# Kernel optimization log

Hardware: AMD Instinct MI355X
Metric: run time of the kernel (lower is better)

Reference implementation:

```python
import jax, jax.numpy as jnp
import numpy as np

INPUT_SIZE = 1024
HEAD_SIZE = 64


def setup_inputs() -> dict:
    key = jax.random.key(0)
    kx, kk, kq, kv = jax.random.split(key, 4)
    B, T, C, H = 4, 4096, INPUT_SIZE, HEAD_SIZE
    x = jax.random.normal(kx, (B, T, C), dtype=jnp.float32)
    # nn.Linear(C, H, bias=False) weight is (H, C); we store transposed (C, H)
    # so that y = x @ W matches torch's x @ weight.T
    scale = 1.0 / np.sqrt(C)
    Wk = jax.random.uniform(kk, (C, H), dtype=jnp.float32, minval=-scale, maxval=scale)
    Wq = jax.random.uniform(kq, (C, H), dtype=jnp.float32, minval=-scale, maxval=scale)
    Wv = jax.random.uniform(kv, (C, H), dtype=jnp.float32, minval=-scale, maxval=scale)
    return {"x": x, "Wk": Wk, "Wq": Wq, "Wv": Wv}


def reference(x, Wk, Wq, Wv):
    B, T, C = x.shape
    k = x @ Wk  # (B, T, H)
    q = x @ Wq
    v = x @ Wv
    H = k.shape[-1]
    # scaled scores (B, T, T)
    wei = jnp.einsum('bth,bsh->bts', q, k) * (H ** -0.5)
    causal = jnp.tril(jnp.ones((T, T), dtype=bool))
    wei = jnp.where(causal, wei, -jnp.inf)
    wei = jax.nn.softmax(wei, axis=-1)
    out = jnp.einsum('bts,bsh->bth', wei, v)  # (B, T, H)
    return out
```

## Files before the change

kernel.cpp:

```cpp
#include <hip/hip_runtime.h>
#include <math.h>


#define BT   16384
#define TDIM 4096
#define CDIM 1024
#define HDIM 64
#define ACCW 68
#define QSCALE 0.18033688f

typedef __attribute__((ext_vector_type(8))) short bf16x8;
typedef __attribute__((ext_vector_type(4))) float f32x4;
typedef __attribute__((ext_vector_type(8))) unsigned short us8;
typedef __attribute__((ext_vector_type(4))) unsigned short us4;

static __device__ __forceinline__ unsigned short f2bf(float f) {
    unsigned int u = __float_as_uint(f);
    u += 0x7fffu + ((u >> 16) & 1u);
    return (unsigned short)(u >> 16);
}

__global__ __launch_bounds__(256) void wtrans(
    const float* __restrict__ Wk, const float* __restrict__ Wq,
    const float* __restrict__ Wv, unsigned short* __restrict__ wtg)
{
    int idx = blockIdx.x * 256 + threadIdx.x;
    int mat = idx >> 16;
    int rem = idx & 65535;
    int h = rem & 63, c = rem >> 6;
    const float* W = (mat == 0) ? Wk : (mat == 1) ? Wq : Wv;
    wtg[(size_t)(mat * 64 + h) * CDIM + c] = f2bf(W[c * HDIM + h]);
}

__global__ __launch_bounds__(512) void qkv_proj(
    const float* __restrict__ x, const unsigned short* __restrict__ wtg,
    unsigned short* __restrict__ kg, unsigned short* __restrict__ qg,
    unsigned short* __restrict__ vtg)
{
    __shared__ __align__(16) unsigned short xs[64][72];
    __shared__ __align__(16) unsigned short wts[192][72];
    const int t = threadIdx.x;
    const int lane = t & 63, wv = t >> 6, quad = lane >> 4, l16 = lane & 15;
    const int mp = wv >> 2;
    const int nq = wv & 3;
    const int row0 = blockIdx.x * 64;

    const int xr0 = t >> 4,      xc4 = (t & 15) * 4;
    const int wn0 = t >> 3,      wc8 = (t & 7) * 8;

    f32x4 acc[2][3];
    #pragma unroll
    for (int i = 0; i < 2; i++)
        #pragma unroll
        for (int j = 0; j < 3; j++) acc[i][j] = (f32x4){0.f, 0.f, 0.f, 0.f};

    float4 xv0 = *(const float4*)&x[(size_t)(row0 + xr0) * CDIM + xc4];
    float4 xv1 = *(const float4*)&x[(size_t)(row0 + xr0 + 32) * CDIM + xc4];
    us8 w0 = *(const us8*)&wtg[(size_t)(wn0 +   0) * CDIM + wc8];
    us8 w1 = *(const us8*)&wtg[(size_t)(wn0 +  64) * CDIM + wc8];
    us8 w2 = *(const us8*)&wtg[(size_t)(wn0 + 128) * CDIM + wc8];

    for (int cc = 0; cc < CDIM; cc += 64) {
        __syncthreads();
        us4 p0 = { f2bf(xv0.x), f2bf(xv0.y), f2bf(xv0.z), f2bf(xv0.w) };
        us4 p1 = { f2bf(xv1.x), f2bf(xv1.y), f2bf(xv1.z), f2bf(xv1.w) };
        *(us4*)&xs[xr0][xc4] = p0;
        *(us4*)&xs[xr0 + 32][xc4] = p1;
        *(us8*)&wts[wn0 +   0][wc8] = w0;
        *(us8*)&wts[wn0 +  64][wc8] = w1;
        *(us8*)&wts[wn0 + 128][wc8] = w2;
        __syncthreads();
        if (cc + 64 < CDIM) {
            int nc = cc + 64;
            xv0 = *(const float4*)&x[(size_t)(row0 + xr0) * CDIM + nc + xc4];
            xv1 = *(const float4*)&x[(size_t)(row0 + xr0 + 32) * CDIM + nc + xc4];
            w0 = *(const us8*)&wtg[(size_t)(wn0 +   0) * CDIM + nc + wc8];
            w1 = *(const us8*)&wtg[(size_t)(wn0 +  64) * CDIM + nc + wc8];
            w2 = *(const us8*)&wtg[(size_t)(wn0 + 128) * CDIM + nc + wc8];
        }
        bf16x8 a[2][2];
        #pragma unroll
        for (int i = 0; i < 2; i++) {
            int mr = (mp * 2 + i) * 16 + l16;
            a[i][0] = *(const bf16x8*)&xs[mr][quad * 8];
            a[i][1] = *(const bf16x8*)&xs[mr][32 + quad * 8];
        }
        #pragma unroll
        for (int j = 0; j < 3; j++) {
            int nt = nq * 3 + j;
            bf16x8 b0 = *(const bf16x8*)&wts[nt * 16 + l16][quad * 8];
            bf16x8 b1 = *(const bf16x8*)&wts[nt * 16 + l16][32 + quad * 8];
            #pragma unroll
            for (int i = 0; i < 2; i++) {
                acc[i][j] = __builtin_amdgcn_mfma_f32_16x16x32_bf16(a[i][0], b0, acc[i][j], 0, 0, 0);
                acc[i][j] = __builtin_amdgcn_mfma_f32_16x16x32_bf16(a[i][1], b1, acc[i][j], 0, 0, 0);
            }
        }
    }

    #pragma unroll
    for (int i = 0; i < 2; i++) {
        const int mrow = row0 + (mp * 2 + i) * 16 + quad * 4;
        #pragma unroll
        for (int j = 0; j < 3; j++) {
            int nt = nq * 3 + j;
            int mat = nt >> 2;
            int col = (nt & 3) * 16 + l16;
            #pragma unroll
            for (int reg = 0; reg < 4; reg++) {
                int r = mrow + reg;
                float val = acc[i][j][reg];
                if (mat == 1) val *= QSCALE;
                unsigned short bv = f2bf(val);
                if (mat == 0)      kg[(size_t)r * HDIM + col] = bv;
                else if (mat == 1) qg[(size_t)r * HDIM + col] = bv;
                else {
                    int bb = r >> 12, tr = r & 4095;
                    vtg[((size_t)(bb * HDIM + col) << 12) + tr] = bv;
                }
            }
        }
    }
}

__global__ __launch_bounds__(256, 3) void attn(
    const unsigned short* __restrict__ qg, const unsigned short* __restrict__ kg,
    const unsigned short* __restrict__ vtg, float* __restrict__ accp)
{
    __shared__ __align__(16) unsigned short Ks[64][72];
    __shared__ __align__(16) unsigned short Vt[80][72];
    __shared__ __align__(16) unsigned short Ps[4][32][72];

    const int t = threadIdx.x;
    const int lane = t & 63, wv = t >> 6, quad = lane >> 4, l16 = lane & 15;

    const int b = blockIdx.x / 144;
    int s = blockIdx.x - b * 144;
    int g = 0;
    while (2 * (g + 1) * (g + 2) <= s) g++;
    int u = s - 2 * g * (g + 1);
    int qi = 4 * g + u / (g + 1);
    int c  = u - (u / (g + 1)) * (g + 1);

    const size_t bbase = (size_t)b * TDIM;
    const int Q0 = qi * 128;
    const int ktmax = 2 * qi + 1;
    const int kt0 = c * 8;
    const int kt1 = (kt0 + 7 < ktmax) ? kt0 + 7 : ktmax;

    for (int i = t; i < 16 * 72; i += 256) {
        int r = i / 72, cc = i - r * 72;
        Vt[64 + r][cc] = (r == 0) ? (unsigned short)0x3F80 : (unsigned short)0;
    }

    const int wrow0 = wv * 32;
    bf16x8 qa[2][2];
    #pragma unroll
    for (int mt2 = 0; mt2 < 2; mt2++) {
        size_t qr = bbase + Q0 + wrow0 + mt2 * 16 + l16;
        qa[mt2][0] = *(const bf16x8*)&qg[qr * HDIM + quad * 8];
        qa[mt2][1] = *(const bf16x8*)&qg[qr * HDIM + 32 + quad * 8];
    }

    f32x4 O[2][5];
    #pragma unroll
    for (int mt2 = 0; mt2 < 2; mt2++)
        #pragma unroll
        for (int i = 0; i < 5; i++) O[mt2][i] = (f32x4){0.f, 0.f, 0.f, 0.f};

    const int fr = t >> 3, fc = (t & 7) * 8;

    us8 kr0 = *(const us8*)&kg[(bbase + kt0 * 64 + fr) * HDIM + fc];
    us8 kr1 = *(const us8*)&kg[(bbase + kt0 * 64 + fr + 32) * HDIM + fc];
    us8 vr0 = *(const us8*)&vtg[((size_t)(b * HDIM + fr) << 12) + kt0 * 64 + fc];
    us8 vr1 = *(const us8*)&vtg[((size_t)(b * HDIM + fr + 32) << 12) + kt0 * 64 + fc];

    for (int kt = kt0; kt <= kt1; kt++) {
        __syncthreads();
        *(us8*)&Ks[fr][fc] = kr0;
        *(us8*)&Ks[fr + 32][fc] = kr1;
        *(us8*)&Vt[fr][fc] = vr0;
        *(us8*)&Vt[fr + 32][fc] = vr1;
        __syncthreads();
        if (kt < kt1) {
            int kn = kt + 1;
            kr0 = *(const us8*)&kg[(bbase + kn * 64 + fr) * HDIM + fc];
            kr1 = *(const us8*)&kg[(bbase + kn * 64 + fr + 32) * HDIM + fc];
            vr0 = *(const us8*)&vtg[((size_t)(b * HDIM + fr) << 12) + kn * 64 + fc];
            vr1 = *(const us8*)&vtg[((size_t)(b * HDIM + fr + 32) << 12) + kn * 64 + fc];
        }

        f32x4 sT[2][4];
        #pragma unroll
        for (int st = 0; st < 4; st++) {
            bf16x8 kb0 = *(const bf16x8*)&Ks[st * 16 + l16][quad * 8];
            bf16x8 kb1 = *(const bf16x8*)&Ks[st * 16 + l16][32 + quad * 8];
            #pragma unroll
            for (int mt2 = 0; mt2 < 2; mt2++) {
                f32x4 z = (f32x4){0.f, 0.f, 0.f, 0.f};
                z = __builtin_amdgcn_mfma_f32_16x16x32_bf16(qa[mt2][0], kb0, z, 0, 0, 0);
                z = __builtin_amdgcn_mfma_f32_16x16x32_bf16(qa[mt2][1], kb1, z, 0, 0, 0);
                sT[mt2][st] = z;
            }
        }
        if (kt * 64 + 63 > Q0 + wrow0) {
            #pragma unroll
            for (int mt2 = 0; mt2 < 2; mt2++)
                #pragma unroll
                for (int st = 0; st < 4; st++) {
                    int gcol = kt * 64 + st * 16 + l16;
                    #pragma unroll
                    for (int r = 0; r < 4; r++) {
                        int grow = Q0 + wrow0 + mt2 * 16 + quad * 4 + r;
                        if (gcol > grow) sT[mt2][st][r] = -1e30f;
                    }
                }
        }
        #pragma unroll
        for (int mt2 = 0; mt2 < 2; mt2++)
            #pragma unroll
            for (int st = 0; st < 4; st++)
                #pragma unroll
                for (int r = 0; r < 4; r++) {
                    float p = exp2f(sT[mt2][st][r]);
                    Ps[wv][mt2 * 16 + quad * 4 + r][st * 16 + l16] = f2bf(p);
                }

        bf16x8 pa[2][2];
        #pragma unroll
        for (int mt2 = 0; mt2 < 2; mt2++) {
            pa[mt2][0] = *(const bf16x8*)&Ps[wv][mt2 * 16 + l16][quad * 8];
            pa[mt2][1] = *(const bf16x8*)&Ps[wv][mt2 * 16 + l16][32 + quad * 8];
        }
        #pragma unroll
        for (int nt = 0; nt < 5; nt++) {
            bf16x8 vb0 = *(const bf16x8*)&Vt[nt * 16 + l16][quad * 8];
            bf16x8 vb1 = *(const bf16x8*)&Vt[nt * 16 + l16][32 + quad * 8];
            #pragma unroll
            for (int mt2 = 0; mt2 < 2; mt2++) {
                O[mt2][nt] = __builtin_amdgcn_mfma_f32_16x16x32_bf16(pa[mt2][0], vb0, O[mt2][nt], 0, 0, 0);
                O[mt2][nt] = __builtin_amdgcn_mfma_f32_16x16x32_bf16(pa[mt2][1], vb1, O[mt2][nt], 0, 0, 0);
            }
        }
    }

    #pragma unroll
    for (int mt2 = 0; mt2 < 2; mt2++) {
        const int grow = (b << 12) + Q0 + wrow0 + mt2 * 16 + quad * 4;
        #pragma unroll
        for (int nt = 0; nt < 4; nt++)
            #pragma unroll
            for (int r = 0; r < 4; r++)
                atomicAdd(&accp[(size_t)(grow + r) * ACCW + nt * 16 + l16], O[mt2][nt][r]);
        if (l16 == 0) {
            #pragma unroll
            for (int r = 0; r < 4; r++)
                atomicAdd(&accp[(size_t)(grow + r) * ACCW + 64], O[mt2][4][r]);
        }
    }
}

__global__ __launch_bounds__(256) void normalize(
    const float* __restrict__ accp, float* __restrict__ out)
{
    int idx = blockIdx.x * 256 + threadIdx.x;
    int row = idx >> 4, c4 = (idx & 15) * 4;
    float inv = 1.f / accp[(size_t)row * ACCW + 64];
    float4 o = *(const float4*)&accp[(size_t)row * ACCW + c4];
    float4 res = make_float4(o.x * inv, o.y * inv, o.z * inv, o.w * inv);
    *(float4*)&out[(size_t)row * HDIM + c4] = res;
}

extern "C" void kernel_launch(void* const* d_in, const int* in_sizes, int n_in,
                              void* d_out, int out_size, void* d_ws, size_t ws_size,
                              hipStream_t stream) {
    const float* x  = (const float*)d_in[0];
    const float* Wk = (const float*)d_in[1];
    const float* Wq = (const float*)d_in[2];
    const float* Wv = (const float*)d_in[3];
    float* out = (float*)d_out;

    unsigned short* wtg = (unsigned short*)d_ws;
    unsigned short* kg  = wtg + 196608;
    unsigned short* qg  = kg + (size_t)BT * HDIM;
    unsigned short* vtg = qg + (size_t)BT * HDIM;
    float* accp = (float*)(vtg + (size_t)4 * HDIM * TDIM);

    hipMemsetAsync(accp, 0, (size_t)BT * ACCW * sizeof(float), stream);
    wtrans<<<768, 256, 0, stream>>>(Wk, Wq, Wv, wtg);
    qkv_proj<<<BT / 64, 512, 0, stream>>>(x, wtg, kg, qg, vtg);
    attn<<<4 * 144, 256, 0, stream>>>(qg, kg, vtg, accp);
    normalize<<<BT * HDIM / (4 * 256), 256, 0, stream>>>(accp, out);
}
```

Baseline: 166.2 us.

## Load K/V fragments directly from global memory and compute row sums in registers

Removes the shared-memory staging of K and V tiles and the two block barriers per key tile, so each wave loads its MFMA operands straight from global memory (relying on L1/L2 for reuse across the four waves). Row sums are now accumulated in registers from the exp values and reduced with shuffles, which drops the ones-column trick and its extra MFMA tile. Each wave also skips key tiles that lie entirely above its own rows, and pairs of bf16 values are packed with the library conversion. The trade is more global and cache traffic per block with no software prefetch, and the occupancy hint is removed.

```diff
diff --git a/kernel.cpp b/kernel.cpp
--- a/kernel.cpp
+++ b/kernel.cpp
@@ -1,4 +1,5 @@
 #include <hip/hip_runtime.h>
+#include <hip/hip_bf16.h>
 #include <math.h>
 
 
@@ -18,6 +19,11 @@
     unsigned int u = __float_as_uint(f);
     u += 0x7fffu + ((u >> 16) & 1u);
     return (unsigned short)(u >> 16);
+}
+
+static __device__ __forceinline__ unsigned int pk2bf(float a, float b) {
+    __hip_bfloat162 h = __float22bfloat162_rn(make_float2(a, b));
+    return *(unsigned int*)&h;
 }
 
 __global__ __launch_bounds__(256) void wtrans(
@@ -123,12 +129,10 @@
     }
 }
 
-__global__ __launch_bounds__(256, 3) void attn(
+__global__ __launch_bounds__(256) void attn(
     const unsigned short* __restrict__ qg, const unsigned short* __restrict__ kg,
     const unsigned short* __restrict__ vtg, float* __restrict__ accp)
 {
-    __shared__ __align__(16) unsigned short Ks[64][72];
-    __shared__ __align__(16) unsigned short Vt[80][72];
     __shared__ __align__(16) unsigned short Ps[4][32][72];
 
     const int t = threadIdx.x;
@@ -144,88 +148,74 @@
 
     const size_t bbase = (size_t)b * TDIM;
     const int Q0 = qi * 128;
-    const int ktmax = 2 * qi + 1;
+    const int wrow0 = wv * 32;
     const int kt0 = c * 8;
-    const int kt1 = (kt0 + 7 < ktmax) ? kt0 + 7 : ktmax;
-
-    for (int i = t; i < 16 * 72; i += 256) {
-        int r = i / 72, cc = i - r * 72;
-        Vt[64 + r][cc] = (r == 0) ? (unsigned short)0x3F80 : (unsigned short)0;
-    }
-
-    const int wrow0 = wv * 32;
+    int kt1 = 2 * qi + 1;
+    int ktw = (Q0 + wrow0 + 31) >> 6;
+    if (ktw < kt1) kt1 = ktw;
+    if (kt0 + 7 < kt1) kt1 = kt0 + 7;
+
     bf16x8 qa[2][2];
     #pragma unroll
     for (int mt2 = 0; mt2 < 2; mt2++) {
-        size_t qr = bbase + Q0 + wrow0 + mt2 * 16 + l16;
-        qa[mt2][0] = *(const bf16x8*)&qg[qr * HDIM + quad * 8];
-        qa[mt2][1] = *(const bf16x8*)&qg[qr * HDIM + 32 + quad * 8];
-    }
-
-    f32x4 O[2][5];
+        const unsigned short* qr = qg + (bbase + Q0 + wrow0 + mt2 * 16 + l16) * HDIM;
+        qa[mt2][0] = *(const bf16x8*)(qr + quad * 8);
+        qa[mt2][1] = *(const bf16x8*)(qr + 32 + quad * 8);
+    }
+
+    f32x4 O[2][4];
     #pragma unroll
     for (int mt2 = 0; mt2 < 2; mt2++)
         #pragma unroll
-        for (int i = 0; i < 5; i++) O[mt2][i] = (f32x4){0.f, 0.f, 0.f, 0.f};
-
-    const int fr = t >> 3, fc = (t & 7) * 8;
-
-    us8 kr0 = *(const us8*)&kg[(bbase + kt0 * 64 + fr) * HDIM + fc];
-    us8 kr1 = *(const us8*)&kg[(bbase + kt0 * 64 + fr + 32) * HDIM + fc];
-    us8 vr0 = *(const us8*)&vtg[((size_t)(b * HDIM + fr) << 12) + kt0 * 64 + fc];
-    us8 vr1 = *(const us8*)&vtg[((size_t)(b * HDIM + fr + 32) << 12) + kt0 * 64 + fc];
+        for (int nt = 0; nt < 4; nt++) O[mt2][nt] = (f32x4){0.f, 0.f, 0.f, 0.f};
+    float lsum[2] = {0.f, 0.f};
+
+    const unsigned short* kbase = kg + bbase * HDIM;
+    const unsigned short* vbase = vtg + (((size_t)b * HDIM) << 12);
 
     for (int kt = kt0; kt <= kt1; kt++) {
-        __syncthreads();
-        *(us8*)&Ks[fr][fc] = kr0;
-        *(us8*)&Ks[fr + 32][fc] = kr1;
-        *(us8*)&Vt[fr][fc] = vr0;
-        *(us8*)&Vt[fr + 32][fc] = vr1;
-        __syncthreads();
-        if (kt < kt1) {
-            int kn = kt + 1;
-            kr0 = *(const us8*)&kg[(bbase + kn * 64 + fr) * HDIM + fc];
-            kr1 = *(const us8*)&kg[(bbase + kn * 64 + fr + 32) * HDIM + fc];
-            vr0 = *(const us8*)&vtg[((size_t)(b * HDIM + fr) << 12) + kn * 64 + fc];
-            vr1 = *(const us8*)&vtg[((size_t)(b * HDIM + fr + 32) << 12) + kn * 64 + fc];
-        }
-
-        f32x4 sT[2][4];
+        bf16x8 ka[4][2];
         #pragma unroll
         for (int st = 0; st < 4; st++) {
-            bf16x8 kb0 = *(const bf16x8*)&Ks[st * 16 + l16][quad * 8];
-            bf16x8 kb1 = *(const bf16x8*)&Ks[st * 16 + l16][32 + quad * 8];
+            const unsigned short* kr = kbase + (size_t)(kt * 64 + st * 16 + l16) * HDIM;
+            ka[st][0] = *(const bf16x8*)(kr + quad * 8);
+            ka[st][1] = *(const bf16x8*)(kr + 32 + quad * 8);
+        }
+        f32x4 sT[4][2];
+        #pragma unroll
+        for (int st = 0; st < 4; st++)
             #pragma unroll
             for (int mt2 = 0; mt2 < 2; mt2++) {
                 f32x4 z = (f32x4){0.f, 0.f, 0.f, 0.f};
-                z = __builtin_amdgcn_mfma_f32_16x16x32_bf16(qa[mt2][0], kb0, z, 0, 0, 0);
-                z = __builtin_amdgcn_mfma_f32_16x16x32_bf16(qa[mt2][1], kb1, z, 0, 0, 0);
-                sT[mt2][st] = z;
-            }
-        }
+                z = __builtin_amdgcn_mfma_f32_16x16x32_bf16(ka[st][0], qa[mt2][0], z, 0, 0, 0);
+                z = __builtin_amdgcn_mfma_f32_16x16x32_bf16(ka[st][1], qa[mt2][1], z, 0, 0, 0);
+                sT[st][mt2] = z;
+            }
         if (kt * 64 + 63 > Q0 + wrow0) {
             #pragma unroll
-            for (int mt2 = 0; mt2 < 2; mt2++)
+            for (int st = 0; st < 4; st++)
                 #pragma unroll
-                for (int st = 0; st < 4; st++) {
-                    int gcol = kt * 64 + st * 16 + l16;
+                for (int mt2 = 0; mt2 < 2; mt2++) {
+                    int qrow = Q0 + wrow0 + mt2 * 16 + l16;
                     #pragma unroll
                     for (int r = 0; r < 4; r++) {
-                        int grow = Q0 + wrow0 + mt2 * 16 + quad * 4 + r;
-                        if (gcol > grow) sT[mt2][st][r] = -1e30f;
+                        int key = kt * 64 + st * 16 + quad * 4 + r;
+                        if (key > qrow) sT[st][mt2][r] = -1e30f;
                     }
                 }
         }
         #pragma unroll
-        for (int mt2 = 0; mt2 < 2; mt2++)
-            #pragma unroll
-            for (int st = 0; st < 4; st++)
-                #pragma unroll
-                for (int r = 0; r < 4; r++) {
-                    float p = exp2f(sT[mt2][st][r]);
-                    Ps[wv][mt2 * 16 + quad * 4 + r][st * 16 + l16] = f2bf(p);
-                }
-
+        for (int st = 0; st < 4; st++)
+            #pragma unroll
+            for (int mt2 = 0; mt2 < 2; mt2++) {
+                float p0 = exp2f(sT[st][mt2][0]);
+                float p1 = exp2f(sT[st][mt2][1]);
+                float p2 = exp2f(sT[st][mt2][2]);
+                float p3 = exp2f(sT[st][mt2][3]);
+                lsum[mt2] += (p0 + p1) + (p2 + p3);
+                uint2 w = make_uint2(pk2bf(p0, p1), pk2bf(p2, p3));
+                *(uint2*)&Ps[wv][mt2 * 16 + l16][st * 16 + quad * 4] = w;
+            }
         bf16x8 pa[2][2];
         #pragma unroll
         for (int mt2 = 0; mt2 < 2; mt2++) {
@@ -233,9 +223,10 @@
             pa[mt2][1] = *(const bf16x8*)&Ps[wv][mt2 * 16 + l16][32 + quad * 8];
         }
         #pragma unroll
-        for (int nt = 0; nt < 5; nt++) {
-            bf16x8 vb0 = *(const bf16x8*)&Vt[nt * 16 + l16][quad * 8];
-            bf16x8 vb1 = *(const bf16x8*)&Vt[nt * 16 + l16][32 + quad * 8];
+        for (int nt = 0; nt < 4; nt++) {
+            const unsigned short* vr = vbase + (((size_t)(nt * 16 + l16)) << 12) + kt * 64;
+            bf16x8 vb0 = *(const bf16x8*)(vr + quad * 8);
+            bf16x8 vb1 = *(const bf16x8*)(vr + 32 + quad * 8);
             #pragma unroll
             for (int mt2 = 0; mt2 < 2; mt2++) {
                 O[mt2][nt] = __builtin_amdgcn_mfma_f32_16x16x32_bf16(pa[mt2][0], vb0, O[mt2][nt], 0, 0, 0);
@@ -246,16 +237,17 @@
 
     #pragma unroll
     for (int mt2 = 0; mt2 < 2; mt2++) {
+        lsum[mt2] += __shfl_xor(lsum[mt2], 16, 64);
+        lsum[mt2] += __shfl_xor(lsum[mt2], 32, 64);
         const int grow = (b << 12) + Q0 + wrow0 + mt2 * 16 + quad * 4;
         #pragma unroll
         for (int nt = 0; nt < 4; nt++)
             #pragma unroll
             for (int r = 0; r < 4; r++)
                 atomicAdd(&accp[(size_t)(grow + r) * ACCW + nt * 16 + l16], O[mt2][nt][r]);
-        if (l16 == 0) {
-            #pragma unroll
-            for (int r = 0; r < 4; r++)
-                atomicAdd(&accp[(size_t)(grow + r) * ACCW + 64], O[mt2][4][r]);
+        if (quad == 0) {
+            int lrow = (b << 12) + Q0 + wrow0 + mt2 * 16 + l16;
+            atomicAdd(&accp[(size_t)lrow * ACCW + 64], lsum[mt2]);
         }
     }
 }
```

New measurement: 188.5 us. 1.13x slower.

## Shrink attention query tile to 64 rows, transpose scores, sum row totals in registers

Applied to the files above, without the earlier changes.

The attention kernel now assigns 64 query rows per block instead of 128, giving twice as many blocks. It computes S^T (keys as the A operand) so each lane holds probabilities for a single query row, and accumulates the softmax denominator in registers with shuffles. This replaces the extra ones-column MFMA tile that the old code appended to V. Per-wave tiles fully above the diagonal are skipped, probabilities are packed with paired bf16 conversion, and the weight transpose kernel now goes through shared memory with vectorized loads and stores. Risks: less reuse of each K/V tile, since it is loaded for fewer queries, and more atomic traffic from the doubled block count.

```diff
diff --git a/kernel.cpp b/kernel.cpp
--- a/kernel.cpp
+++ b/kernel.cpp
@@ -1,4 +1,5 @@
 #include <hip/hip_runtime.h>
+#include <hip/hip_bf16.h>
 #include <math.h>
 
 
@@ -20,16 +21,38 @@
     return (unsigned short)(u >> 16);
 }
 
+static __device__ __forceinline__ unsigned int pk2bf(float a, float b) {
+    __hip_bfloat162 h = __float22bfloat162_rn(make_float2(a, b));
+    return *(unsigned int*)&h;
+}
+
 __global__ __launch_bounds__(256) void wtrans(
     const float* __restrict__ Wk, const float* __restrict__ Wq,
     const float* __restrict__ Wv, unsigned short* __restrict__ wtg)
 {
-    int idx = blockIdx.x * 256 + threadIdx.x;
-    int mat = idx >> 16;
-    int rem = idx & 65535;
-    int h = rem & 63, c = rem >> 6;
+    __shared__ float tile[64][65];
+    const int mat = blockIdx.x >> 4, ct = blockIdx.x & 15;
     const float* W = (mat == 0) ? Wk : (mat == 1) ? Wq : Wv;
-    wtg[(size_t)(mat * 64 + h) * CDIM + c] = f2bf(W[c * HDIM + h]);
+    const int c0 = ct * 64;
+    const int t = threadIdx.x;
+    #pragma unroll
+    for (int p = 0; p < 4; p++) {
+        int idx = p * 256 + t;
+        int c = idx >> 4, h4 = (idx & 15) * 4;
+        float4 v = *(const float4*)&W[(size_t)(c0 + c) * HDIM + h4];
+        tile[c][h4] = v.x; tile[c][h4 + 1] = v.y;
+        tile[c][h4 + 2] = v.z; tile[c][h4 + 3] = v.w;
+    }
+    __syncthreads();
+    #pragma unroll
+    for (int p = 0; p < 2; p++) {
+        int idx = p * 256 + t;
+        int h = idx >> 3, c8 = (idx & 7) * 8;
+        us8 o;
+        #pragma unroll
+        for (int j = 0; j < 8; j++) o[j] = f2bf(tile[c8 + j][h]);
+        *(us8*)&wtg[(size_t)(mat * 64 + h) * CDIM + c0 + c8] = o;
+    }
 }
 
 __global__ __launch_bounds__(512) void qkv_proj(
@@ -123,50 +146,39 @@
     }
 }
 
-__global__ __launch_bounds__(256, 3) void attn(
+__global__ __launch_bounds__(256) void attn(
     const unsigned short* __restrict__ qg, const unsigned short* __restrict__ kg,
     const unsigned short* __restrict__ vtg, float* __restrict__ accp)
 {
     __shared__ __align__(16) unsigned short Ks[64][72];
-    __shared__ __align__(16) unsigned short Vt[80][72];
-    __shared__ __align__(16) unsigned short Ps[4][32][72];
+    __shared__ __align__(16) unsigned short Vt[64][72];
+    __shared__ __align__(16) unsigned short Ps[4][16][72];
 
     const int t = threadIdx.x;
     const int lane = t & 63, wv = t >> 6, quad = lane >> 4, l16 = lane & 15;
 
-    const int b = blockIdx.x / 144;
-    int s = blockIdx.x - b * 144;
+    const int b = blockIdx.x / 288;
+    int s = blockIdx.x - b * 288;
     int g = 0;
-    while (2 * (g + 1) * (g + 2) <= s) g++;
-    int u = s - 2 * g * (g + 1);
-    int qi = 4 * g + u / (g + 1);
+    while (4 * (g + 1) * (g + 2) <= s) g++;
+    int u = s - 4 * g * (g + 1);
+    int qt = 8 * g + u / (g + 1);
     int c  = u - (u / (g + 1)) * (g + 1);
 
     const size_t bbase = (size_t)b * TDIM;
-    const int Q0 = qi * 128;
-    const int ktmax = 2 * qi + 1;
+    const int Q0 = qt * 64;
     const int kt0 = c * 8;
-    const int kt1 = (kt0 + 7 < ktmax) ? kt0 + 7 : ktmax;
-
-    for (int i = t; i < 16 * 72; i += 256) {
-        int r = i / 72, cc = i - r * 72;
-        Vt[64 + r][cc] = (r == 0) ? (unsigned short)0x3F80 : (unsigned short)0;
-    }
-
-    const int wrow0 = wv * 32;
-    bf16x8 qa[2][2];
-    #pragma unroll
-    for (int mt2 = 0; mt2 < 2; mt2++) {
-        size_t qr = bbase + Q0 + wrow0 + mt2 * 16 + l16;
-        qa[mt2][0] = *(const bf16x8*)&qg[qr * HDIM + quad * 8];
-        qa[mt2][1] = *(const bf16x8*)&qg[qr * HDIM + 32 + quad * 8];
-    }
-
-    f32x4 O[2][5];
-    #pragma unroll
-    for (int mt2 = 0; mt2 < 2; mt2++)
-        #pragma unroll
-        for (int i = 0; i < 5; i++) O[mt2][i] = (f32x4){0.f, 0.f, 0.f, 0.f};
+    const int kt1 = (kt0 + 7 < qt) ? kt0 + 7 : qt;
+
+    const int qrow = Q0 + wv * 16 + l16;
+    const unsigned short* qr = qg + (bbase + qrow) * HDIM;
+    bf16x8 qa0 = *(const bf16x8*)(qr + quad * 8);
+    bf16x8 qa1 = *(const bf16x8*)(qr + 32 + quad * 8);
+
+    f32x4 O[4];
+    #pragma unroll
+    for (int nt = 0; nt < 4; nt++) O[nt] = (f32x4){0.f, 0.f, 0.f, 0.f};
+    float lsum = 0.f;
 
     const int fr = t >> 3, fc = (t & 7) * 8;
 
@@ -174,6 +186,8 @@
     us8 kr1 = *(const us8*)&kg[(bbase + kt0 * 64 + fr + 32) * HDIM + fc];
     us8 vr0 = *(const us8*)&vtg[((size_t)(b * HDIM + fr) << 12) + kt0 * 64 + fc];
     us8 vr1 = *(const us8*)&vtg[((size_t)(b * HDIM + fr + 32) << 12) + kt0 * 64 + fc];
+
+    const int wlast = Q0 + wv * 16 + 15;
 
     for (int kt = kt0; kt <= kt1; kt++) {
         __syncthreads();
@@ -189,75 +203,58 @@
             vr0 = *(const us8*)&vtg[((size_t)(b * HDIM + fr) << 12) + kn * 64 + fc];
             vr1 = *(const us8*)&vtg[((size_t)(b * HDIM + fr + 32) << 12) + kn * 64 + fc];
         }
-
-        f32x4 sT[2][4];
+        if (kt * 64 > wlast) continue;
+
+        f32x4 sT[4];
         #pragma unroll
         for (int st = 0; st < 4; st++) {
-            bf16x8 kb0 = *(const bf16x8*)&Ks[st * 16 + l16][quad * 8];
-            bf16x8 kb1 = *(const bf16x8*)&Ks[st * 16 + l16][32 + quad * 8];
-            #pragma unroll
-            for (int mt2 = 0; mt2 < 2; mt2++) {
-                f32x4 z = (f32x4){0.f, 0.f, 0.f, 0.f};
-                z = __builtin_amdgcn_mfma_f32_16x16x32_bf16(qa[mt2][0], kb0, z, 0, 0, 0);
-                z = __builtin_amdgcn_mfma_f32_16x16x32_bf16(qa[mt2][1], kb1, z, 0, 0, 0);
-                sT[mt2][st] = z;
-            }
-        }
-        if (kt * 64 + 63 > Q0 + wrow0) {
-            #pragma unroll
-            for (int mt2 = 0; mt2 < 2; mt2++)
-                #pragma unroll
-                for (int st = 0; st < 4; st++) {
-                    int gcol = kt * 64 + st * 16 + l16;
-                    #pragma unroll
-                    for (int r = 0; r < 4; r++) {
-                        int grow = Q0 + wrow0 + mt2 * 16 + quad * 4 + r;
-                        if (gcol > grow) sT[mt2][st][r] = -1e30f;
-                    }
-                }
-        }
-        #pragma unroll
-        for (int mt2 = 0; mt2 < 2; mt2++)
+            bf16x8 ka0 = *(const bf16x8*)&Ks[st * 16 + l16][quad * 8];
+            bf16x8 ka1 = *(const bf16x8*)&Ks[st * 16 + l16][32 + quad * 8];
+            f32x4 z = (f32x4){0.f, 0.f, 0.f, 0.f};
+            z = __builtin_amdgcn_mfma_f32_16x16x32_bf16(ka0, qa0, z, 0, 0, 0);
+            z = __builtin_amdgcn_mfma_f32_16x16x32_bf16(ka1, qa1, z, 0, 0, 0);
+            sT[st] = z;
+        }
+        if (kt * 64 + 63 > Q0 + wv * 16) {
             #pragma unroll
             for (int st = 0; st < 4; st++)
                 #pragma unroll
                 for (int r = 0; r < 4; r++) {
-                    float p = exp2f(sT[mt2][st][r]);
-                    Ps[wv][mt2 * 16 + quad * 4 + r][st * 16 + l16] = f2bf(p);
+                    int key = kt * 64 + st * 16 + quad * 4 + r;
+                    if (key > qrow) sT[st][r] = -1e30f;
                 }
-
-        bf16x8 pa[2][2];
-        #pragma unroll
-        for (int mt2 = 0; mt2 < 2; mt2++) {
-            pa[mt2][0] = *(const bf16x8*)&Ps[wv][mt2 * 16 + l16][quad * 8];
-            pa[mt2][1] = *(const bf16x8*)&Ps[wv][mt2 * 16 + l16][32 + quad * 8];
-        }
-        #pragma unroll
-        for (int nt = 0; nt < 5; nt++) {
+        }
+        #pragma unroll
+        for (int st = 0; st < 4; st++) {
+            float p0 = exp2f(sT[st][0]);
+            float p1 = exp2f(sT[st][1]);
+            float p2 = exp2f(sT[st][2]);
+            float p3 = exp2f(sT[st][3]);
+            lsum += (p0 + p1) + (p2 + p3);
+            uint2 w = make_uint2(pk2bf(p0, p1), pk2bf(p2, p3));
+            *(uint2*)&Ps[wv][l16][st * 16 + quad * 4] = w;
+        }
+        bf16x8 pa0 = *(const bf16x8*)&Ps[wv][l16][quad * 8];
+        bf16x8 pa1 = *(const bf16x8*)&Ps[wv][l16][32 + quad * 8];
+        #pragma unroll
+        for (int nt = 0; nt < 4; nt++) {
             bf16x8 vb0 = *(const bf16x8*)&Vt[nt * 16 + l16][quad * 8];
             bf16x8 vb1 = *(const bf16x8*)&Vt[nt * 16 + l16][32 + quad * 8];
-            #pragma unroll
-            for (int mt2 = 0; mt2 < 2; mt2++) {
-                O[mt2][nt] = __builtin_amdgcn_mfma_f32_16x16x32_bf16(pa[mt2][0], vb0, O[mt2][nt], 0, 0, 0);
-                O[mt2][nt] = __builtin_amdgcn_mfma_f32_16x16x32_bf16(pa[mt2][1], vb1, O[mt2][nt], 0, 0, 0);
-            }
-        }
-    }
-
-    #pragma unroll
-    for (int mt2 = 0; mt2 < 2; mt2++) {
-        const int grow = (b << 12) + Q0 + wrow0 + mt2 * 16 + quad * 4;
-        #pragma unroll
-        for (int nt = 0; nt < 4; nt++)
-            #pragma unroll
-            for (int r = 0; r < 4; r++)
-                atomicAdd(&accp[(size_t)(grow + r) * ACCW + nt * 16 + l16], O[mt2][nt][r]);
-        if (l16 == 0) {
-            #pragma unroll
-            for (int r = 0; r < 4; r++)
-                atomicAdd(&accp[(size_t)(grow + r) * ACCW + 64], O[mt2][4][r]);
-        }
-    }
+            O[nt] = __builtin_amdgcn_mfma_f32_16x16x32_bf16(pa0, vb0, O[nt], 0, 0, 0);
+            O[nt] = __builtin_amdgcn_mfma_f32_16x16x32_bf16(pa1, vb1, O[nt], 0, 0, 0);
+        }
+    }
+
+    lsum += __shfl_xor(lsum, 16, 64);
+    lsum += __shfl_xor(lsum, 32, 64);
+    const int grow = (b << 12) + Q0 + wv * 16 + quad * 4;
+    #pragma unroll
+    for (int nt = 0; nt < 4; nt++)
+        #pragma unroll
+        for (int r = 0; r < 4; r++)
+            atomicAdd(&accp[(size_t)(grow + r) * ACCW + nt * 16 + l16], O[nt][r]);
+    if (quad == 0)
+        atomicAdd(&accp[(size_t)((b << 12) + qrow) * ACCW + 64], lsum);
 }
 
 __global__ __launch_bounds__(256) void normalize(
@@ -287,8 +284,8 @@
     float* accp = (float*)(vtg + (size_t)4 * HDIM * TDIM);
 
     hipMemsetAsync(accp, 0, (size_t)BT * ACCW * sizeof(float), stream);
-    wtrans<<<768, 256, 0, stream>>>(Wk, Wq, Wv, wtg);
+    wtrans<<<48, 256, 0, stream>>>(Wk, Wq, Wv, wtg);
     qkv_proj<<<BT / 64, 512, 0, stream>>>(x, wtg, kg, qg, vtg);
-    attn<<<4 * 144, 256, 0, stream>>>(qg, kg, vtg, accp);
+    attn<<<4 * 288, 256, 0, stream>>>(qg, kg, vtg, accp);
     normalize<<<BT * HDIM / (4 * 256), 256, 0, stream>>>(accp, out);
 }
```

Result: faster. 160.6 us (-3.3%).
